# Optimization experiments

Hardware: AMD Instinct MI355X
Metric: run time of the kernel (lower is better)

## Reference

```python
import jax, jax.numpy as jnp
import numpy as np

B, S, V, D, H, DK, DFF, L = 2, 1024, 513, 512, 8, 64, 2048, 6
PAD_IDX = -1.0
EPS_GPE = 0.1

def _sinusoid_table(n_position, d_hid):
    pos = np.arange(n_position)[:, None].astype(np.float64)
    i = np.arange(d_hid)[None, :]
    angle = pos / np.power(10000.0, 2 * (i // 2) / d_hid)
    tab = np.zeros((n_position, d_hid), dtype=np.float32)
    tab[:, 0::2] = np.sin(angle[:, 0::2])
    tab[:, 1::2] = np.cos(angle[:, 1::2])
    return jnp.asarray(tab)

_POS_TABLE = _sinusoid_table(2048, D)

def _ln(x, g, b, eps=1e-6):
    m = x.mean(-1, keepdims=True)
    v = x.var(-1, keepdims=True)
    return (x - m) * jax.lax.rsqrt(v + eps) * g + b

def _mha(x_q, x_kv, wq_, wk_, wv_, wo_, mask, g, b):
    Bq, Sq, _ = x_q.shape
    Skv = x_kv.shape[1]
    q = (x_q @ wq_).reshape(Bq, Sq, H, DK).transpose(0, 2, 1, 3)
    k = (x_kv @ wk_).reshape(Bq, Skv, H, DK).transpose(0, 2, 1, 3)
    v = (x_kv @ wv_).reshape(Bq, Skv, H, DK).transpose(0, 2, 1, 3)
    scores = jnp.einsum('bhqd,bhkd->bhqk', q, k) / np.float32(np.sqrt(DK))
    scores = jnp.where(mask[:, None], scores, jnp.float32(-1e9))
    attn = jax.nn.softmax(scores, axis=-1)
    out = jnp.einsum('bhqk,bhkd->bhqd', attn, v).transpose(0, 2, 1, 3).reshape(Bq, Sq, D)
    return _ln(x_q + out @ wo_, g, b)

def _forward(dec_in, prev_dec_out, trg, adj, graph_length, gr_mask, gr_pos_enc_kernel,
             emb_w1, emb_b1, emb_w2, emb_b2, emb_w3, emb_b3, ln0_g, ln0_b,
             wq, wk, wv, wo, ln1_g, ln1_b,
             cq, ck, cv, co, ln2_g, ln2_b,
             ffn_w1, ffn_b1, ffn_w2, ffn_b2, ln3_g, ln3_b,
             p_w1, p_b1, p_w2, p_b2, p_w3, p_b3):
    # masks (n_ensemble = 1 so dec_in[:, :, 0, :] == dec_in)
    causal = jnp.tril(jnp.ones((S, S), bool))
    slf_mask = jnp.all(dec_in != PAD_IDX, -1)[:, None, :] & causal          # [B,S,S]
    enc_mask = jnp.all(prev_dec_out != PAD_IDX, -1)[:, None, :]             # [B,1,S]
    # word-embedding MLP: 513 -> 513 -> 513 -> 512
    h = jax.nn.relu(dec_in @ emb_w1 + emb_b1)
    h = jax.nn.relu(h @ emb_w2 + emb_b2)
    h = h @ emb_w3 + emb_b3                                                 # [B,S,D]
    # propagation graph positional encoding (k = 0..2, un-normalized branch)
    w = (1.0 - EPS_GPE) ** jnp.arange(gr_pos_enc_kernel.shape[1], dtype=jnp.float32)
    base = _POS_TABLE[:S]                                                   # [S,D]
    emb = jnp.einsum('k,bkst,td->bsd', w, gr_pos_enc_kernel, base) / w.sum()
    h = _ln(h + emb, ln0_g, ln0_b)
    for i in range(L):
        h = _mha(h, h, wq[i], wk[i], wv[i], wo[i], slf_mask, ln1_g[i], ln1_b[i])
        h = _mha(h, prev_dec_out, cq[i], ck[i], cv[i], co[i], enc_mask, ln2_g[i], ln2_b[i])
        f = jax.nn.relu(h @ ffn_w1[i] + ffn_b1[i]) @ ffn_w2[i] + ffn_b2[i]
        h = _ln(h + f, ln3_g[i], ln3_b[i])
    # projection head: 512 -> 513 -> 513 -> 513
    z = jax.nn.relu(h @ p_w1 + p_b1)
    z = jax.nn.relu(z @ p_w2 + p_b2)
    return z @ p_w3 + p_b3                                                  # [B,S,V]

def setup_inputs():
    key = jax.random.key(0)
    ks = jax.random.split(key, 24)
    def xavier(k, shape):
        lim = np.float32(np.sqrt(6.0 / (shape[-2] + shape[-1])))
        return jax.random.uniform(k, shape, jnp.float32, -lim, lim)
    inp = {}
    inp['dec_in'] = jax.random.uniform(ks[0], (B, S, V), jnp.float32)
    inp['prev_dec_out'] = jax.random.normal(ks[1], (B, S, D), jnp.float32)
    inp['trg'] = jnp.zeros((B, S, V), jnp.float32)
    inp['adj'] = jnp.zeros((B, S, S), jnp.float32)
    inp['graph_length'] = jnp.zeros((B, S, 10), jnp.float32)
    inp['gr_mask'] = jnp.zeros((B, 1, S, S), jnp.float32)
    gk = jax.random.uniform(ks[2], (B, 3, S, S), jnp.float32)
    inp['gr_pos_enc_kernel'] = gk / jnp.sum(gk, -1, keepdims=True)  # row-stochastic diffusion kernels
    SZ = max(V, D)  # sz_intermed = 513
    inp['emb_w1'] = xavier(ks[3], (V, SZ)); inp['emb_b1'] = jnp.zeros((SZ,))
    inp['emb_w2'] = xavier(ks[4], (SZ, SZ)); inp['emb_b2'] = jnp.zeros((SZ,))
    inp['emb_w3'] = xavier(ks[5], (SZ, D)); inp['emb_b3'] = jnp.zeros((D,))
    inp['ln0_g'] = jnp.ones((D,)); inp['ln0_b'] = jnp.zeros((D,))
    for name, ki, shp in [('wq', 6, (L, D, D)), ('wk', 7, (L, D, D)), ('wv', 8, (L, D, D)), ('wo', 9, (L, D, D)),
                          ('cq', 10, (L, D, D)), ('ck', 11, (L, D, D)), ('cv', 12, (L, D, D)), ('co', 13, (L, D, D)),
                          ('ffn_w1', 14, (L, D, DFF)), ('ffn_w2', 15, (L, DFF, D))]:
        inp[name] = xavier(ks[ki], shp)
    inp['ffn_b1'] = jnp.zeros((L, DFF)); inp['ffn_b2'] = jnp.zeros((L, D))
    inp['ln1_g'] = jnp.ones((L, D)); inp['ln1_b'] = jnp.zeros((L, D))
    inp['ln2_g'] = jnp.ones((L, D)); inp['ln2_b'] = jnp.zeros((L, D))
    inp['ln3_g'] = jnp.ones((L, D)); inp['ln3_b'] = jnp.zeros((L, D))
    inp['p_w1'] = xavier(ks[16], (D, V)); inp['p_b1'] = jnp.zeros((V,))
    inp['p_w2'] = xavier(ks[17], (V, V)); inp['p_b2'] = jnp.zeros((V,))
    inp['p_w3'] = xavier(ks[18], (V, V)); inp['p_b3'] = jnp.zeros((V,))
    return inp

def reference(dec_in, prev_dec_out, trg, adj, graph_length, gr_mask, gr_pos_enc_kernel,
              emb_w1, emb_b1, emb_w2, emb_b2, emb_w3, emb_b3, ln0_g, ln0_b,
              wq, wk, wv, wo, ln1_g, ln1_b,
              cq, ck, cv, co, ln2_g, ln2_b,
              ffn_w1, ffn_b1, ffn_w2, ffn_b2, ln3_g, ln3_b,
              p_w1, p_b1, p_w2, p_b2, p_w3, p_b3):
    return _forward(dec_in, prev_dec_out, trg, adj, graph_length, gr_mask, gr_pos_enc_kernel,
                    emb_w1, emb_b1, emb_w2, emb_b2, emb_w3, emb_b3, ln0_g, ln0_b,
                    wq, wk, wv, wo, ln1_g, ln1_b,
                    cq, ck, cv, co, ln2_g, ln2_b,
                    ffn_w1, ffn_b1, ffn_w2, ffn_b2, ln3_g, ln3_b,
                    p_w1, p_b1, p_w2, p_b2, p_w3, p_b3)
```

## Files before the change

kernel.cpp:

```cpp
#include <hip/hip_runtime.h>
#include <hip/hip_bf16.h>
#include <stdint.h>

#define BB 2
#define SS 1024
#define VV 513
#define VP 576
#define DD 512
#define HH 8
#define DKK 64
#define DFFN 2048
#define LL 6
#define MM (BB * SS)

typedef __bf16 bf16x8 __attribute__((ext_vector_type(8)));
typedef float f32x4 __attribute__((ext_vector_type(4)));
typedef unsigned short us8 __attribute__((ext_vector_type(8)));
typedef unsigned short us4 __attribute__((ext_vector_type(4)));

static __device__ inline unsigned short f2bf(float f) {
  union { float f; unsigned u; } v; v.f = f;
  unsigned u = v.u;
  unsigned r = (u + 0x7FFFu + ((u >> 16) & 1u)) >> 16;
  return (unsigned short)r;
}

static __device__ inline bf16x8 ldfrag(const unsigned short* p) {
  us8 r = *(const us8*)p;
  return __builtin_bit_cast(bf16x8, r);
}

typedef __attribute__((address_space(3))) void lds_void;
typedef const __attribute__((address_space(1))) void glb_void;
static __device__ inline void gl_lds16(const void* g, void* l) {
  __builtin_amdgcn_global_load_lds((glb_void*)g, (lds_void*)l, 16, 0, 0);
}

static __device__ inline bf16x8 ldfrag_swz(const unsigned short* base, int row, int kloc) {
  const unsigned byte = (unsigned)(row * 128 + kloc * 2) ^ (unsigned)((row & 7) << 4);
  return ldfrag((const unsigned short*)((const char*)base + byte));
}

static __device__ inline int rot3(int x) { return (x == 2) ? 0 : x + 1; }

struct GemmP {
  const unsigned short* A;
  const unsigned short* B0; const unsigned short* B1; const unsigned short* B2;
  const float* bias;
  float* C;
  unsigned short* D0; unsigned short* D1; unsigned short* D2;
  int Kp, Np, ldc, Nreal, relu;
};

template<int NB, int NT, int TRV, int KS>
__global__ __launch_bounds__(256)
void gemm_tpl(GemmP p)
{
  constexpr int FN = NT / 32;
  __shared__ unsigned short Al[3][64 * 64];
  __shared__ unsigned short Bl[3][NT * 64];
  const int tid = threadIdx.x;
  const int l = tid & 63, w = tid >> 6;
  const int wm = w >> 1, wn = w & 1;
  const int lr = l & 15, lg = l >> 4;

  const int nbn = p.Np / NT;
  int sel = 0, bx = blockIdx.x;
  if (NB > 1) { sel = bx / nbn; bx -= sel * nbn; }
  const unsigned short* Bmat = p.B0;
  if (NB > 1 && sel == 1) Bmat = p.B1;
  if (NB > 2 && sel == 2) Bmat = p.B2;
  const int m0 = blockIdx.y << 6, n0 = bx * NT;
  const int kz = (KS > 1) ? blockIdx.z : 0;

  f32x4 acc[2][FN];
  const f32x4 zf = {0.f, 0.f, 0.f, 0.f};
#pragma unroll
  for (int i = 0; i < 2; ++i)
#pragma unroll
    for (int j = 0; j < FN; ++j) acc[i][j] = zf;

  const size_t Kp = (size_t)p.Kp;
  const unsigned short* Abase = p.A + (size_t)m0 * Kp;
  const unsigned short* Bbase = Bmat + (size_t)n0 * Kp;
  const int nt = (p.Kp >> 6) / KS;
  const int kb0 = kz * nt;

  auto stage = [&](int buf, int kt) {
    const int k0 = (kb0 + kt) << 6;
#pragma unroll
    for (int j = 0; j < 2; ++j) {
      const int ti = j * 256 + tid;
      const int row = ti >> 3;
      const int ch = (ti & 7) ^ (row & 7);
      gl_lds16(Abase + (size_t)row * Kp + k0 + ch * 8, &Al[buf][ti * 8]);
    }
#pragma unroll
    for (int j = 0; j < FN; ++j) {
      const int ti = j * 256 + tid;
      const int row = ti >> 3;
      const int ch = (ti & 7) ^ (row & 7);
      gl_lds16(Bbase + (size_t)row * Kp + k0 + ch * 8, &Bl[buf][ti * 8]);
    }
  };

  stage(0, 0);
  if (nt > 1) stage(1, 1);
  int cb = 0, sb = 2;

  for (int kt = 0; kt < nt; ++kt) {
    if (kt + 1 < nt) {
      if constexpr (FN == 2) asm volatile("s_waitcnt vmcnt(4)" ::: "memory");
      else                   asm volatile("s_waitcnt vmcnt(6)" ::: "memory");
    } else {
      asm volatile("s_waitcnt vmcnt(0)" ::: "memory");
    }
    __builtin_amdgcn_s_barrier();
    if (kt + 2 < nt) { stage(sb, kt + 2); sb = rot3(sb); }
#pragma unroll
    for (int ks = 0; ks < 2; ++ks) {
      bf16x8 af[2], bfv[FN];
#pragma unroll
      for (int mf = 0; mf < 2; ++mf)
        af[mf] = ldfrag_swz(Al[cb], wm * 32 + mf * 16 + lr, ks * 32 + lg * 8);
#pragma unroll
      for (int nf = 0; nf < FN; ++nf)
        bfv[nf] = ldfrag_swz(Bl[cb], wn * (NT / 2) + nf * 16 + lr, ks * 32 + lg * 8);
#pragma unroll
      for (int mf = 0; mf < 2; ++mf)
#pragma unroll
        for (int nf = 0; nf < FN; ++nf)
          acc[mf][nf] = __builtin_amdgcn_mfma_f32_16x16x32_bf16(af[mf], bfv[nf], acc[mf][nf], 0, 0, 0);
    }
    cb = rot3(cb);
  }

  unsigned short* Dsel = p.D0;
  if (NB > 1 && sel == 1) Dsel = p.D1;
  if (NB > 2 && sel == 2) Dsel = p.D2;

  if (TRV && sel == 2) {
#pragma unroll
    for (int mf = 0; mf < 2; ++mf) {
      const int growb = m0 + wm * 32 + mf * 16 + (lg << 2);
      const int b = growb >> 10, s = growb & 1023;
#pragma unroll
      for (int nf = 0; nf < FN; ++nf) {
        const int gcol = n0 + wn * (NT / 2) + nf * 16 + lr;
        const int h = gcol >> 6, d = gcol & 63;
        us4 t;
#pragma unroll
        for (int r = 0; r < 4; ++r) t[r] = f2bf(acc[mf][nf][r]);
        *(us4*)(Dsel + (((size_t)(b * HH) + h) * DKK + d) * SS + s) = t;
      }
    }
    return;
  }

  float* Cz = p.C ? (p.C + (size_t)kz * MM * p.ldc) : nullptr;
#pragma unroll
  for (int mf = 0; mf < 2; ++mf) {
#pragma unroll
    for (int r = 0; r < 4; ++r) {
      const int grow = m0 + wm * 32 + mf * 16 + (lg << 2) + r;
#pragma unroll
      for (int nf = 0; nf < FN; ++nf) {
        const int gcol = n0 + wn * (NT / 2) + nf * 16 + lr;
        float v = acc[mf][nf][r];
        if (p.bias && kz == 0 && gcol < p.Nreal) v += p.bias[gcol];
        if (p.relu) v = fmaxf(v, 0.f);
        if (Dsel) Dsel[(size_t)grow * p.Np + gcol] = f2bf(v);
        if (Cz && gcol < p.Nreal) Cz[(size_t)grow * p.ldc + gcol] = v;
      }
    }
  }
}

struct GemmBat {
  const unsigned short* A;
  const unsigned short* B[12];
  unsigned short* D[12];
  int Kp, Np;
};

__global__ __launch_bounds__(256)
void gemm_bat(GemmBat p)
{
  __shared__ unsigned short Al[3][64 * 64];
  __shared__ unsigned short Bl[3][64 * 64];
  const int tid = threadIdx.x;
  const int l = tid & 63, w = tid >> 6;
  const int wm = w >> 1, wn = w & 1;
  const int lr = l & 15, lg = l >> 4;

  const int nbn = p.Np >> 6;
  const int sel = blockIdx.x / nbn;
  const int bx = blockIdx.x - sel * nbn;
  const unsigned short* Bmat = p.B[sel];
  unsigned short* Dmat = p.D[sel];
  const int m0 = blockIdx.y << 6, n0 = bx << 6;

  f32x4 acc[2][2];
  const f32x4 zf = {0.f, 0.f, 0.f, 0.f};
#pragma unroll
  for (int i = 0; i < 2; ++i)
#pragma unroll
    for (int j = 0; j < 2; ++j) acc[i][j] = zf;

  const size_t Kp = (size_t)p.Kp;
  const unsigned short* Abase = p.A + (size_t)m0 * Kp;
  const unsigned short* Bbase = Bmat + (size_t)n0 * Kp;

  auto stage = [&](int buf, int kt) {
    const int k0 = kt << 6;
#pragma unroll
    for (int j = 0; j < 2; ++j) {
      const int ti = j * 256 + tid;
      const int row = ti >> 3;
      const int ch = (ti & 7) ^ (row & 7);
      gl_lds16(Abase + (size_t)row * Kp + k0 + ch * 8, &Al[buf][ti * 8]);
    }
#pragma unroll
    for (int j = 0; j < 2; ++j) {
      const int ti = j * 256 + tid;
      const int row = ti >> 3;
      const int ch = (ti & 7) ^ (row & 7);
      gl_lds16(Bbase + (size_t)row * Kp + k0 + ch * 8, &Bl[buf][ti * 8]);
    }
  };

  const int nt = p.Kp >> 6;
  stage(0, 0);
  if (nt > 1) stage(1, 1);
  int cb = 0, sb = 2;

  for (int kt = 0; kt < nt; ++kt) {
    if (kt + 1 < nt) asm volatile("s_waitcnt vmcnt(4)" ::: "memory");
    else             asm volatile("s_waitcnt vmcnt(0)" ::: "memory");
    __builtin_amdgcn_s_barrier();
    if (kt + 2 < nt) { stage(sb, kt + 2); sb = rot3(sb); }
#pragma unroll
    for (int ks = 0; ks < 2; ++ks) {
      bf16x8 af[2], bfv[2];
#pragma unroll
      for (int mf = 0; mf < 2; ++mf)
        af[mf] = ldfrag_swz(Al[cb], wm * 32 + mf * 16 + lr, ks * 32 + lg * 8);
#pragma unroll
      for (int nf = 0; nf < 2; ++nf)
        bfv[nf] = ldfrag_swz(Bl[cb], wn * 32 + nf * 16 + lr, ks * 32 + lg * 8);
#pragma unroll
      for (int mf = 0; mf < 2; ++mf)
#pragma unroll
        for (int nf = 0; nf < 2; ++nf)
          acc[mf][nf] = __builtin_amdgcn_mfma_f32_16x16x32_bf16(af[mf], bfv[nf], acc[mf][nf], 0, 0, 0);
    }
    cb = rot3(cb);
  }

  if (sel & 1) {
#pragma unroll
    for (int mf = 0; mf < 2; ++mf) {
      const int growb = m0 + wm * 32 + mf * 16 + (lg << 2);
      const int b = growb >> 10, s = growb & 1023;
#pragma unroll
      for (int nf = 0; nf < 2; ++nf) {
        const int gcol = n0 + wn * 32 + nf * 16 + lr;
        const int h = gcol >> 6, d = gcol & 63;
        us4 t;
#pragma unroll
        for (int r = 0; r < 4; ++r) t[r] = f2bf(acc[mf][nf][r]);
        *(us4*)(Dmat + (((size_t)(b * HH) + h) * DKK + d) * SS + s) = t;
      }
    }
    return;
  }

#pragma unroll
  for (int mf = 0; mf < 2; ++mf) {
#pragma unroll
    for (int r = 0; r < 4; ++r) {
      const int grow = m0 + wm * 32 + mf * 16 + (lg << 2) + r;
#pragma unroll
      for (int nf = 0; nf < 2; ++nf) {
        const int gcol = n0 + wn * 32 + nf * 16 + lr;
        Dmat[(size_t)grow * p.Np + gcol] = f2bf(acc[mf][nf][r]);
      }
    }
  }
}

__global__ __launch_bounds__(128)
void attn_kernel(const unsigned short* __restrict__ Qb,
                 const unsigned short* __restrict__ Kb,
                 const unsigned short* __restrict__ VbT,
                 unsigned short* __restrict__ Ob,
                 const float* __restrict__ maskadd)
{
  __shared__ unsigned short Kl[2][2][64 * 64];
  __shared__ unsigned short Vl[2][2][64 * 64];
  __shared__ char PC[9216];
  unsigned short* Pl = (unsigned short*)PC;
  float (*comb)[66] = (float(*)[66])PC;

  const int tid = threadIdx.x;
  const int l = tid & 63, w = tid >> 6;
  const int qt = blockIdx.x, h = blockIdx.y, b = blockIdx.z;
  const int lr = l & 15, lg = l >> 4;

  bf16x8 qf[2][2];
#pragma unroll
  for (int mf = 0; mf < 2; ++mf) {
    const unsigned short* qrow = Qb + ((size_t)(b * SS) + qt * 32 + mf * 16 + lr) * DD + h * DKK;
    qf[mf][0] = ldfrag(qrow + (lg << 3));
    qf[mf][1] = ldfrag(qrow + 32 + (lg << 3));
  }

  const unsigned short* Kbase = Kb + (size_t)(b * SS) * DD + h * DKK;
  const unsigned short* Vbase = VbT + ((size_t)(b * HH) + h) * DKK * SS;

  auto stage = [&](int buf, int kt) {
#pragma unroll
    for (int j = 0; j < 8; ++j) {
      const int ti = j * 64 + l;
      const int row = ti >> 3;
      const int ch = (ti & 7) ^ (row & 7);
      gl_lds16(Kbase + (size_t)(kt * 64 + row) * DD + ch * 8, &Kl[w][buf][ti * 8]);
    }
#pragma unroll
    for (int j = 0; j < 8; ++j) {
      const int ti = j * 64 + l;
      const int row = ti >> 3;
      const int ch = (ti & 7) ^ (row & 7);
      gl_lds16(Vbase + (size_t)row * SS + kt * 64 + ch * 8, &Vl[w][buf][ti * 8]);
    }
  };

  f32x4 accO[2][4];
  const f32x4 zf = {0.f, 0.f, 0.f, 0.f};
#pragma unroll
  for (int mf = 0; mf < 2; ++mf)
#pragma unroll
    for (int nf = 0; nf < 4; ++nf) accO[mf][nf] = zf;
  float mold[2][4], lsum[2][4];
#pragma unroll
  for (int mf = 0; mf < 2; ++mf)
#pragma unroll
    for (int r = 0; r < 4; ++r) { mold[mf][r] = -1e30f; lsum[mf][r] = 0.f; }

  const int ktmax = (qt >> 1) + 1;
  const int myn = (ktmax - w + 1) >> 1;

  if (myn > 0) stage(0, w);
  int buf = 0;

  for (int i = 0; i < myn; ++i) {
    const int kt = w + 2 * i;
    if (i + 1 < myn) {
      stage(buf ^ 1, kt + 2);
      asm volatile("s_waitcnt vmcnt(16)" ::: "memory");
    } else {
      asm volatile("s_waitcnt vmcnt(0)" ::: "memory");
    }
    const unsigned short* KB = &Kl[w][buf][0];
    const unsigned short* VB = &Vl[w][buf][0];
    float sc[2][4][4];
    __builtin_amdgcn_s_setprio(1);
#pragma unroll
    for (int nf = 0; nf < 4; ++nf) {
      bf16x8 k0 = ldfrag_swz(KB, nf * 16 + lr, lg * 8);
      bf16x8 k1 = ldfrag_swz(KB, nf * 16 + lr, 32 + lg * 8);
// ... 309 lines not shown
        accO[mf][nf] = __builtin_amdgcn_mfma_f32_16x16x32_bf16(pa[mf][1], v1, accO[mf][nf], 0, 0, 0);
      }
    }
    __builtin_amdgcn_s_setprio(0);
    buf ^= 1;
  }

  __syncthreads();
  if (w == 1) {
#pragma unroll
    for (int mf = 0; mf < 2; ++mf)
#pragma unroll
      for (int r = 0; r < 4; ++r) {
        const int qrow = mf * 16 + (lg << 2) + r;
#pragma unroll
        for (int nf = 0; nf < 4; ++nf)
          comb[qrow][nf * 16 + lr] = accO[mf][nf][r];
        if (lr == 0) { comb[qrow][64] = mold[mf][r]; comb[qrow][65] = lsum[mf][r]; }
      }
  }
  __syncthreads();
  if (w == 0) {
#pragma unroll
    for (int mf = 0; mf < 2; ++mf)
#pragma unroll
      for (int r = 0; r < 4; ++r) {
        const int qrow = mf * 16 + (lg << 2) + r;
        const float m1 = comb[qrow][64], l1 = comb[qrow][65];
        const float m0v = mold[mf][r], l0 = lsum[mf][r];
        const float ms = fmaxf(m0v, m1);
        const float f0 = __expf(m0v - ms), f1 = __expf(m1 - ms);
        const float inv = 1.f / (l0 * f0 + l1 * f1);
        const size_t orow = ((size_t)(b * SS) + qt * 32 + mf * 16 + (lg << 2) + r) * DD + h * DKK;
#pragma unroll
        for (int nf = 0; nf < 4; ++nf)
          Ob[orow + nf * 16 + lr] =
              f2bf((accO[mf][nf][r] * f0 + comb[qrow][nf * 16 + lr] * f1) * inv);
      }
  }
}

template<int P>
__global__ __launch_bounds__(256)
void addln_kernel(const float* __restrict__ a, const float* __restrict__ c,
                  const float* __restrict__ g, const float* __restrict__ bb,
                  float* __restrict__ hf, unsigned short* __restrict__ hb)
{
  const int row = blockIdx.x * 4 + (threadIdx.x >> 6);
  const int l = threadIdx.x & 63;
  const float* ar = a + (size_t)row * DD + l * 8;
  f32x4 x0 = *(const f32x4*)ar;
  f32x4 x1 = *(const f32x4*)(ar + 4);
#pragma unroll
  for (int pp = 0; pp < P; ++pp) {
    const float* cr = c + (size_t)pp * MM * DD + (size_t)row * DD + l * 8;
    x0 += *(const f32x4*)cr;
    x1 += *(const f32x4*)(cr + 4);
  }
  float sum = x0[0] + x0[1] + x0[2] + x0[3] + x1[0] + x1[1] + x1[2] + x1[3];
#pragma unroll
  for (int off = 1; off < 64; off <<= 1) sum += __shfl_xor(sum, off, 64);
  const float mean = sum * (1.f / 512.f);
  float vs = 0.f;
#pragma unroll
  for (int j = 0; j < 4; ++j) { float d0 = x0[j] - mean; float d1 = x1[j] - mean; vs += d0 * d0 + d1 * d1; }
#pragma unroll
  for (int off = 1; off < 64; off <<= 1) vs += __shfl_xor(vs, off, 64);
  const float rs = rsqrtf(vs * (1.f / 512.f) + 1e-6f);
  const f32x4 g0 = *(const f32x4*)(g + l * 8), g1 = *(const f32x4*)(g + l * 8 + 4);
  const f32x4 b0 = *(const f32x4*)(bb + l * 8), b1 = *(const f32x4*)(bb + l * 8 + 4);
  f32x4 o0, o1;
  us8 ob;
#pragma unroll
  for (int j = 0; j < 4; ++j) {
    o0[j] = (x0[j] - mean) * rs * g0[j] + b0[j];
    o1[j] = (x1[j] - mean) * rs * g1[j] + b1[j];
    ob[j] = f2bf(o0[j]); ob[j + 4] = f2bf(o1[j]);
  }
  float* of = hf + (size_t)row * DD + l * 8;
  *(f32x4*)of = o0; *(f32x4*)(of + 4) = o1;
  *(us8*)(hb + (size_t)row * DD + l * 8) = ob;
}

__global__ __launch_bounds__(256)
void prep_all(const float* __restrict__ dec_in, const float* __restrict__ prev,
              unsigned short* __restrict__ decb, unsigned short* __restrict__ prevb,
              float* __restrict__ kvs, float* __restrict__ kve,
              unsigned short* __restrict__ tabT,
              const float* __restrict__ gk, unsigned short* __restrict__ Mb)
{
  const int blk = blockIdx.x, tid = threadIdx.x;
  if (blk < 1024) {
    const int isdec = blk < 512;
    const int row = (isdec ? blk : blk - 512) * 4 + (tid >> 6);
    const int l = tid & 63;
    const int NC = isdec ? VV : DD, NP = isdec ? VP : DD;
    const float* xr = (isdec ? dec_in : prev) + (size_t)row * NC;
    unsigned short* ob = (isdec ? decb : prevb) + (size_t)row * NP;
    int ok = 1;
    for (int j = l; j < NP; j += 64) {
      if (j < NC) {
        const float v = xr[j];
        ok &= (v != -1.0f) ? 1 : 0;
        ob[j] = f2bf(v);
      } else ob[j] = 0;
    }
    ok = __all(ok) ? 1 : 0;
    if (l == 0) (isdec ? kvs : kve)[row] = ok ? 0.f : -1e9f;
  } else if (blk < 3072) {
    const int i = (blk - 1024) * 256 + tid;
    const int d = i >> 10, s = i & 1023;
    const float ex = (float)(2 * (d >> 1)) * (1.0f / (float)DD);
    const float ang = (float)s * exp2f(ex * -13.287712379549449f);
    tabT[i] = f2bf((d & 1) ? cosf(ang) : sinf(ang));
  } else {
    const int i = (blk - 3072) * 256 + tid;
    const int b = i / (SS * SS);
    const int rem = i - b * (SS * SS);
    const float* p = gk + (size_t)b * 3 * SS * SS + rem;
    Mb[i] = f2bf((p[0] + 0.9f * p[SS * SS] + 0.81f * p[2 * SS * SS]) * (1.0f / 2.71f));
  }
}

struct WJobs {
  const float* W[8]; unsigned short* WT[8];
  int K[8], N[8], Kp[8], Np[8], nbx[8], nby[8];
  int off[9];
};
__global__ __launch_bounds__(256)
void wconv_all(WJobs p)
{
  __shared__ float t[64][65];
  const int bid = blockIdx.x;
  int j = 0;
#pragma unroll
  for (int i = 0; i < 8; ++i) if (bid >= p.off[i + 1]) j = i + 1;
  const int local = bid - p.off[j];
  const int per = p.nbx[j] * p.nby[j];
  const int z = local / per;
  const int rem = local - z * per;
  const int by = rem / p.nbx[j];
  const int bx = rem - by * p.nbx[j];
  const int K = p.K[j], N = p.N[j], Kp = p.Kp[j], Np = p.Np[j];
  const float* Wl = p.W[j] + (size_t)z * K * N;
  unsigned short* WTl = p.WT[j] + (size_t)z * Np * Kp;
  const int n0 = bx << 6, k0 = by << 6;
  const int cx = threadIdx.x & 63, ry = threadIdx.x >> 6;
#pragma unroll
  for (int i = 0; i < 16; ++i) {
    const int kk = k0 + ry + i * 4, nn = n0 + cx;
    t[ry + i * 4][cx] = (kk < K && nn < N) ? Wl[(size_t)kk * N + nn] : 0.f;
  }
  __syncthreads();
#pragma unroll
  for (int i = 0; i < 16; ++i) {
    const int nn = n0 + ry + i * 4, kk = k0 + cx;
    if (nn < Np && kk < Kp) WTl[(size_t)nn * Kp + kk] = f2bf(t[cx][ry + i * 4]);
  }
}

struct WconvB { const float* W[8]; unsigned short* WT[8]; };
__global__ __launch_bounds__(256)
void wconv8_kernel(WconvB p)
{
  __shared__ float t[64][65];
  const int z = blockIdx.z;
  const int wi = z / LL, li = z - wi * LL;
  const float* Wl = p.W[wi] + (size_t)li * DD * DD;
  unsigned short* WTl = p.WT[wi] + (size_t)li * DD * DD;
  const int n0 = blockIdx.x << 6, k0 = blockIdx.y << 6;
  const int cx = threadIdx.x & 63, ry = threadIdx.x >> 6;
#pragma unroll
  for (int i = 0; i < 16; ++i)
    t[ry + i * 4][cx] = Wl[(size_t)(k0 + ry + i * 4) * DD + n0 + cx];
  __syncthreads();
#pragma unroll
  for (int i = 0; i < 16; ++i)
    WTl[(size_t)(n0 + ry + i * 4) * DD + k0 + cx] = f2bf(t[cx][ry + i * 4]);
}

static inline void g1(hipStream_t s, const unsigned short* A, const unsigned short* B,
                      const float* bias, float* C, unsigned short* D,
                      int Kp, int Np, int ldc, int Nreal, int relu)
{
  GemmP p{};
  p.A = A; p.B0 = B; p.bias = bias; p.C = C; p.D0 = D;
  p.Kp = Kp; p.Np = Np; p.ldc = ldc; p.Nreal = Nreal; p.relu = relu;
  gemm_tpl<1, 64, 0, 1><<<dim3(Np >> 6, MM >> 6), 256, 0, s>>>(p);
}

static inline void g1w(hipStream_t s, const unsigned short* A, const unsigned short* B,
                       const float* bias, unsigned short* D, int Kp, int Np, int relu)
{
  GemmP p{};
  p.A = A; p.B0 = B; p.bias = bias; p.D0 = D;
  p.Kp = Kp; p.Np = Np; p.ldc = Np; p.Nreal = Np; p.relu = relu;
  gemm_tpl<1, 128, 0, 1><<<dim3(Np >> 7, MM >> 6), 256, 0, s>>>(p);
}

template<int KS>
static inline void g1k(hipStream_t s, const unsigned short* A, const unsigned short* B,
                       const float* bias, float* C, int Kp)
{
  GemmP p{};
  p.A = A; p.B0 = B; p.bias = bias; p.C = C;
  p.Kp = Kp; p.Np = DD; p.ldc = DD; p.Nreal = DD; p.relu = 0;
  gemm_tpl<1, 64, 0, KS><<<dim3(DD >> 6, MM >> 6, KS), 256, 0, s>>>(p);
}

static inline void g3t(hipStream_t s, const unsigned short* A, const unsigned short* B0,
                       const unsigned short* B1, const unsigned short* B2,
                       unsigned short* D0, unsigned short* D1, unsigned short* D2T)
{
  GemmP p{};
  p.A = A; p.B0 = B0; p.B1 = B1; p.B2 = B2; p.D0 = D0; p.D1 = D1; p.D2 = D2T;
  p.Kp = DD; p.Np = DD; p.ldc = DD; p.Nreal = DD; p.relu = 0;
  gemm_tpl<3, 64, 1, 1><<<dim3(3 * (DD >> 6), MM >> 6), 256, 0, s>>>(p);
}

extern "C" void kernel_launch(void* const* d_in, const int* in_sizes, int n_in,
                              void* d_out, int out_size, void* d_ws, size_t ws_size,
                              hipStream_t stream)
{
  (void)in_sizes; (void)n_in; (void)out_size; (void)ws_size;
  const float* dec_in = (const float*)d_in[0];
  const float* prev   = (const float*)d_in[1];
  const float* gk     = (const float*)d_in[6];
  const float* emb_w1 = (const float*)d_in[7];
  const float* emb_b1 = (const float*)d_in[8];
  const float* emb_w2 = (const float*)d_in[9];
  const float* emb_b2 = (const float*)d_in[10];
  const float* emb_w3 = (const float*)d_in[11];
  const float* emb_b3 = (const float*)d_in[12];
  const float* ln0_g  = (const float*)d_in[13];
  const float* ln0_b  = (const float*)d_in[14];
  const float* wq     = (const float*)d_in[15];
  const float* wk     = (const float*)d_in[16];
  const float* wv     = (const float*)d_in[17];
  const float* wo     = (const float*)d_in[18];
  const float* cq     = (const float*)d_in[19];
  const float* ck     = (const float*)d_in[20];
  const float* cv     = (const float*)d_in[21];
  const float* co     = (const float*)d_in[22];
  const float* ffn_w1 = (const float*)d_in[23];
  const float* ffn_w2 = (const float*)d_in[24];
  const float* ffn_b1 = (const float*)d_in[25];
  const float* ffn_b2 = (const float*)d_in[26];
  const float* ln1_g  = (const float*)d_in[27];
  const float* ln1_b  = (const float*)d_in[28];
  const float* ln2_g  = (const float*)d_in[29];
  const float* ln2_b  = (const float*)d_in[30];
  const float* ln3_g  = (const float*)d_in[31];
  const float* ln3_b  = (const float*)d_in[32];
  const float* p_w1   = (const float*)d_in[33];
  const float* p_b1   = (const float*)d_in[34];
  const float* p_w2   = (const float*)d_in[35];
  const float* p_b2   = (const float*)d_in[36];
  const float* p_w3   = (const float*)d_in[37];
  const float* p_b3   = (const float*)d_in[38];

  char* wsp = (char*)d_ws;
  auto carve = [&](size_t bytes) { char* r = wsp; wsp += (bytes + 255) & ~(size_t)255; return r; };

  unsigned short* decb  = (unsigned short*)carve((size_t)MM * VP * 2);
  unsigned short* prevb = (unsigned short*)carve((size_t)MM * DD * 2);
  float*          hf    = (float*)carve((size_t)MM * DD * 4);
  unsigned short* hb    = (unsigned short*)carve((size_t)MM * DD * 2);
  float*          xf1   = (float*)carve((size_t)MM * DD * 4);
  unsigned short* tb1   = (unsigned short*)carve((size_t)MM * DFFN * 2);
  unsigned short* Mbb   = tb1;
  float*          xf2   = (float*)((char*)tb1 + (size_t)MM * SS * 2);
  unsigned short* tb2a  = (unsigned short*)carve((size_t)MM * VP * 2);
  unsigned short* tb2b  = (unsigned short*)carve((size_t)MM * VP * 2);
  unsigned short* qb    = (unsigned short*)carve((size_t)MM * DD * 2);
  unsigned short* kb    = (unsigned short*)carve((size_t)MM * DD * 2);
  unsigned short* vbT   = (unsigned short*)carve((size_t)MM * DD * 2);
  float* kvs = (float*)carve((size_t)MM * 4);
  float* kve = (float*)carve((size_t)MM * 4);
  unsigned short* postabt = (unsigned short*)carve((size_t)DD * SS * 2);
  unsigned short* ew1t  = (unsigned short*)carve((size_t)VP * VP * 2);
  unsigned short* ew2t  = (unsigned short*)carve((size_t)VP * VP * 2);
  unsigned short* ew3t  = (unsigned short*)carve((size_t)DD * VP * 2);
  unsigned short* wqt   = (unsigned short*)carve((size_t)LL * DD * DD * 2);
  unsigned short* wkt   = (unsigned short*)carve((size_t)LL * DD * DD * 2);
  unsigned short* wvt   = (unsigned short*)carve((size_t)LL * DD * DD * 2);
  unsigned short* wot   = (unsigned short*)carve((size_t)LL * DD * DD * 2);
  unsigned short* cqt   = (unsigned short*)carve((size_t)LL * DD * DD * 2);
  unsigned short* ckt   = (unsigned short*)carve((size_t)LL * DD * DD * 2);
  unsigned short* cvt   = (unsigned short*)carve((size_t)LL * DD * DD * 2);
  unsigned short* cot   = (unsigned short*)carve((size_t)LL * DD * DD * 2);
  unsigned short* f1t   = (unsigned short*)carve((size_t)LL * DFFN * DD * 2);
  unsigned short* f2t   = (unsigned short*)carve((size_t)LL * DD * DFFN * 2);
  unsigned short* p1t   = (unsigned short*)carve((size_t)VP * DD * 2);
  unsigned short* p2t   = (unsigned short*)carve((size_t)VP * VP * 2);
  unsigned short* p3t   = (unsigned short*)carve((size_t)VP * VP * 2);
  unsigned short* ckall = (unsigned short*)carve((size_t)LL * MM * DD * 2);
  unsigned short* cvbT  = (unsigned short*)carve((size_t)LL * MM * DD * 2);
  float*          xk4   = (float*)carve((size_t)4 * MM * DD * 4);

  const dim3 agrid(SS / 32, HH, BB);

  prep_all<<<11264, 256, 0, stream>>>(dec_in, prev, decb, prevb, kvs, kve, postabt, gk, Mbb);

  {
    WconvB wb{};
    wb.W[0] = wq; wb.W[1] = wk; wb.W[2] = wv; wb.W[3] = wo;
    wb.W[4] = cq; wb.W[5] = ck; wb.W[6] = cv; wb.W[7] = co;
    wb.WT[0] = wqt; wb.WT[1] = wkt; wb.WT[2] = wvt; wb.WT[3] = wot;
    wb.WT[4] = cqt; wb.WT[5] = ckt; wb.WT[6] = cvt; wb.WT[7] = cot;
    wconv8_kernel<<<dim3(8, 8, 8 * LL), 256, 0, stream>>>(wb);
  }
  {
    WJobs wj{};
    const float* Ws[8]   = {emb_w1, emb_w2, emb_w3, ffn_w1, ffn_w2, p_w1, p_w2, p_w3};
    unsigned short* Ds[8] = {ew1t, ew2t, ew3t, f1t, f2t, p1t, p2t, p3t};
    const int Ks[8]  = {VV, VV, VV, DD, DFFN, DD, VV, VV};
    const int Ns[8]  = {VV, VV, DD, DFFN, DD, VV, VV, VV};
    const int Kps[8] = {VP, VP, VP, DD, DFFN, DD, VP, VP};
    const int Nps[8] = {VP, VP, DD, DFFN, DD, VP, VP, VP};
    const int nls[8] = {1, 1, 1, LL, LL, 1, 1, 1};
    int off = 0;
    for (int j = 0; j < 8; ++j) {
      wj.W[j] = Ws[j]; wj.WT[j] = Ds[j];
      wj.K[j] = Ks[j]; wj.N[j] = Ns[j]; wj.Kp[j] = Kps[j]; wj.Np[j] = Nps[j];
      wj.nbx[j] = (Nps[j] + 63) / 64; wj.nby[j] = (Kps[j] + 63) / 64;
      wj.off[j] = off;
      off += wj.nbx[j] * wj.nby[j] * nls[j];
    }
    wj.off[8] = off;
    wconv_all<<<off, 256, 0, stream>>>(wj);
  }

  {
    GemmBat p{};
    p.A = prevb; p.Kp = DD; p.Np = DD;
    for (int i = 0; i < LL; ++i) {
      p.B[2 * i]     = ckt + (size_t)i * DD * DD;
      p.B[2 * i + 1] = cvt + (size_t)i * DD * DD;
      p.D[2 * i]     = ckall + (size_t)i * MM * DD;
      p.D[2 * i + 1] = cvbT + (size_t)i * MM * DD;
    }
    gemm_bat<<<dim3(12 * (DD >> 6), MM >> 6), 256, 0, stream>>>(p);
  }

  g1(stream, decb, ew1t, emb_b1, nullptr, tb2a, VP, VP, VP, VV, 1);
  g1(stream, tb2a, ew2t, emb_b2, nullptr, tb2b, VP, VP, VP, VV, 1);
  g1(stream, tb2b, ew3t, emb_b3, xf1, nullptr, VP, DD, DD, DD, 0);
  g1(stream, Mbb, postabt, nullptr, xf2, nullptr, SS, DD, DD, DD, 0);
  addln_kernel<1><<<MM / 4, 256, 0, stream>>>(xf1, xf2, ln0_g, ln0_b, hf, hb);

  for (int i = 0; i < LL; ++i) {
    const size_t od = (size_t)i * DD * DD;
    g3t(stream, hb, wqt + od, wkt + od, wvt + od, qb, kb, vbT);
    attn_kernel<<<agrid, 128, 0, stream>>>(qb, kb, vbT, qb, kvs);
    g1k<2>(stream, qb, wot + od, nullptr, xk4, DD);
    addln_kernel<2><<<MM / 4, 256, 0, stream>>>(hf, xk4, ln1_g + i * DD, ln1_b + i * DD, hf, hb);
    attnx_kernel<<<agrid, 128, 0, stream>>>(hb, cqt + od, ckall + (size_t)i * MM * DD,
                                            cvbT + (size_t)i * MM * DD, qb, kve);
    g1k<2>(stream, qb, cot + od, nullptr, xk4, DD);
    addln_kernel<2><<<MM / 4, 256, 0, stream>>>(hf, xk4, ln2_g + i * DD, ln2_b + i * DD, hf, hb);
    g1w(stream, hb, f1t + (size_t)i * DFFN * DD, ffn_b1 + i * DFFN, tb1, DD, DFFN, 1);
    g1k<4>(stream, tb1, f2t + (size_t)i * DD * DFFN, ffn_b2 + i * DD, xk4, DFFN);
    addln_kernel<4><<<MM / 4, 256, 0, stream>>>(hf, xk4, ln3_g + i * DD, ln3_b + i * DD, hf, hb);
  }

  g1(stream, hb, p1t, p_b1, nullptr, tb2a, DD, VP, VP, VV, 1);
  g1(stream, tb2a, p2t, p_b2, nullptr, tb2b, VP, VP, VP, VV, 1);
  g1(stream, tb2b, p3t, p_b3, (float*)d_out, nullptr, VP, VP, VV, VV, 0);
}
```

Baseline: 994.0 us.

## Merge prologue kernels and batch independent startup GEMMs into one launch

The input prep, positional table, graph-kernel mix and both weight-transpose kernels are combined into a single prologue launch with block-range dispatch. The cross-attention K/V batch GEMM, the first embedding GEMM and the positional-encoding GEMM are also merged into one multi-job GEMM launch, since they are mutually independent. The aim is to cut launch overhead and the idle gaps at each kernel tail. The cost is a larger shared-memory footprint on every prologue block and hard-coded block counts that assume these exact shapes.

```diff
diff --git a/kernel.cpp b/kernel.cpp
--- a/kernel.cpp
+++ b/kernel.cpp
@@ -43,6 +43,61 @@
 
 static __device__ inline int rot3(int x) { return (x == 2) ? 0 : x + 1; }
 
+__device__ __forceinline__ void gemm_core64(
+    unsigned short* Al, unsigned short* Bl,
+    const unsigned short* Abase, const unsigned short* Bbase, int Kp, int nt,
+    f32x4 (&acc)[2][2])
+{
+  const int tid = threadIdx.x;
+  const int l = tid & 63, w = tid >> 6;
+  const int wm = w >> 1, wn = w & 1;
+  const int lr = l & 15, lg = l >> 4;
+
+  auto stage = [&](int buf, int kt) {
+    const int k0 = kt << 6;
+#pragma unroll
+    for (int j = 0; j < 2; ++j) {
+      const int ti = j * 256 + tid;
+      const int row = ti >> 3;
+      const int ch = (ti & 7) ^ (row & 7);
+      gl_lds16(Abase + (size_t)row * Kp + k0 + ch * 8, &Al[buf * 4096 + ti * 8]);
+    }
+#pragma unroll
+    for (int j = 0; j < 2; ++j) {
+      const int ti = j * 256 + tid;
+      const int row = ti >> 3;
+      const int ch = (ti & 7) ^ (row & 7);
+      gl_lds16(Bbase + (size_t)row * Kp + k0 + ch * 8, &Bl[buf * 4096 + ti * 8]);
+    }
+  };
+
+  stage(0, 0);
+  if (nt > 1) stage(1, 1);
+  int cb = 0, sb = 2;
+  for (int kt = 0; kt < nt; ++kt) {
+    if (kt + 1 < nt) asm volatile("s_waitcnt vmcnt(4)" ::: "memory");
+    else             asm volatile("s_waitcnt vmcnt(0)" ::: "memory");
+    __builtin_amdgcn_s_barrier();
+    if (kt + 2 < nt) { stage(sb, kt + 2); sb = rot3(sb); }
+#pragma unroll
+    for (int ks = 0; ks < 2; ++ks) {
+      bf16x8 af[2], bfv[2];
+#pragma unroll
+      for (int mf = 0; mf < 2; ++mf)
+        af[mf] = ldfrag_swz(Al + cb * 4096, wm * 32 + mf * 16 + lr, ks * 32 + lg * 8);
+#pragma unroll
+      for (int nf = 0; nf < 2; ++nf)
+        bfv[nf] = ldfrag_swz(Bl + cb * 4096, wn * 32 + nf * 16 + lr, ks * 32 + lg * 8);
+#pragma unroll
+      for (int mf = 0; mf < 2; ++mf)
+#pragma unroll
+        for (int nf = 0; nf < 2; ++nf)
+          acc[mf][nf] = __builtin_amdgcn_mfma_f32_16x16x32_bf16(af[mf], bfv[nf], acc[mf][nf], 0, 0, 0);
+    }
+    cb = rot3(cb);
+  }
+}
+
 struct GemmP {
   const unsigned short* A;
   const unsigned short* B0; const unsigned short* B1; const unsigned short* B2;
@@ -176,116 +231,102 @@
   }
 }
 
-struct GemmBat {
+struct GemmMultiP {
   const unsigned short* A;
   const unsigned short* B[12];
   unsigned short* D[12];
-  int Kp, Np;
+  const unsigned short* eA; const unsigned short* eB; const float* ebias;
+  unsigned short* eD;
+  const unsigned short* gA; const unsigned short* gB; float* gC;
 };
 
 __global__ __launch_bounds__(256)
-void gemm_bat(GemmBat p)
-{
-  __shared__ unsigned short Al[3][64 * 64];
-  __shared__ unsigned short Bl[3][64 * 64];
+void gemm_multi(GemmMultiP p)
+{
+  __shared__ unsigned short Al[3 * 4096];
+  __shared__ unsigned short Bl[3 * 4096];
+  const int bid = blockIdx.x;
   const int tid = threadIdx.x;
   const int l = tid & 63, w = tid >> 6;
   const int wm = w >> 1, wn = w & 1;
   const int lr = l & 15, lg = l >> 4;
-
-  const int nbn = p.Np >> 6;
-  const int sel = blockIdx.x / nbn;
-  const int bx = blockIdx.x - sel * nbn;
-  const unsigned short* Bmat = p.B[sel];
-  unsigned short* Dmat = p.D[sel];
-  const int m0 = blockIdx.y << 6, n0 = bx << 6;
-
+  const f32x4 zf = {0.f, 0.f, 0.f, 0.f};
   f32x4 acc[2][2];
-  const f32x4 zf = {0.f, 0.f, 0.f, 0.f};
 #pragma unroll
   for (int i = 0; i < 2; ++i)
 #pragma unroll
     for (int j = 0; j < 2; ++j) acc[i][j] = zf;
 
-  const size_t Kp = (size_t)p.Kp;
-  const unsigned short* Abase = p.A + (size_t)m0 * Kp;
-  const unsigned short* Bbase = Bmat + (size_t)n0 * Kp;
-
-  auto stage = [&](int buf, int kt) {
-    const int k0 = kt << 6;
-#pragma unroll
-    for (int j = 0; j < 2; ++j) {
-      const int ti = j * 256 + tid;
-      const int row = ti >> 3;
-      const int ch = (ti & 7) ^ (row & 7);
-      gl_lds16(Abase + (size_t)row * Kp + k0 + ch * 8, &Al[buf][ti * 8]);
-    }
-#pragma unroll
-    for (int j = 0; j < 2; ++j) {
-      const int ti = j * 256 + tid;
-      const int row = ti >> 3;
-      const int ch = (ti & 7) ^ (row & 7);
-      gl_lds16(Bbase + (size_t)row * Kp + k0 + ch * 8, &Bl[buf][ti * 8]);
-    }
-  };
-
-  const int nt = p.Kp >> 6;
-  stage(0, 0);
-  if (nt > 1) stage(1, 1);
-  int cb = 0, sb = 2;
-
-  for (int kt = 0; kt < nt; ++kt) {
-    if (kt + 1 < nt) asm volatile("s_waitcnt vmcnt(4)" ::: "memory");
-    else             asm volatile("s_waitcnt vmcnt(0)" ::: "memory");
-    __builtin_amdgcn_s_barrier();
-    if (kt + 2 < nt) { stage(sb, kt + 2); sb = rot3(sb); }
-#pragma unroll
-    for (int ks = 0; ks < 2; ++ks) {
-      bf16x8 af[2], bfv[2];
+  if (bid < 3072) {
+    const int sel = bid >> 8;
+    const int rem = bid & 255;
+    const int by = rem >> 3, bx = rem & 7;
+    const int m0 = by << 6, n0 = bx << 6;
+    gemm_core64(Al, Bl, p.A + (size_t)m0 * DD, p.B[sel] + (size_t)n0 * DD, DD, 8, acc);
+    unsigned short* Dmat = p.D[sel];
+    if (sel & 1) {
+#pragma unroll
+      for (int mf = 0; mf < 2; ++mf) {
+        const int growb = m0 + wm * 32 + mf * 16 + (lg << 2);
+        const int b = growb >> 10, s = growb & 1023;
+#pragma unroll
+        for (int nf = 0; nf < 2; ++nf) {
+          const int gcol = n0 + wn * 32 + nf * 16 + lr;
+          const int h = gcol >> 6, d = gcol & 63;
+          us4 t;
+#pragma unroll
+          for (int r = 0; r < 4; ++r) t[r] = f2bf(acc[mf][nf][r]);
+          *(us4*)(Dmat + (((size_t)(b * HH) + h) * DKK + d) * SS + s) = t;
+        }
+      }
+    } else {
 #pragma unroll
       for (int mf = 0; mf < 2; ++mf)
-        af[mf] = ldfrag_swz(Al[cb], wm * 32 + mf * 16 + lr, ks * 32 + lg * 8);
-#pragma unroll
-      for (int nf = 0; nf < 2; ++nf)
-        bfv[nf] = ldfrag_swz(Bl[cb], wn * 32 + nf * 16 + lr, ks * 32 + lg * 8);
-#pragma unroll
-      for (int mf = 0; mf < 2; ++mf)
-#pragma unroll
-        for (int nf = 0; nf < 2; ++nf)
-          acc[mf][nf] = __builtin_amdgcn_mfma_f32_16x16x32_bf16(af[mf], bfv[nf], acc[mf][nf], 0, 0, 0);
-    }
-    cb = rot3(cb);
-  }
-
-  if (sel & 1) {
-#pragma unroll
-    for (int mf = 0; mf < 2; ++mf) {
-      const int growb = m0 + wm * 32 + mf * 16 + (lg << 2);
-      const int b = growb >> 10, s = growb & 1023;
-#pragma unroll
-      for (int nf = 0; nf < 2; ++nf) {
-        const int gcol = n0 + wn * 32 + nf * 16 + lr;
-        const int h = gcol >> 6, d = gcol & 63;
-        us4 t;
-#pragma unroll
-        for (int r = 0; r < 4; ++r) t[r] = f2bf(acc[mf][nf][r]);
-        *(us4*)(Dmat + (((size_t)(b * HH) + h) * DKK + d) * SS + s) = t;
-      }
-    }
-    return;
-  }
-
-#pragma unroll
-  for (int mf = 0; mf < 2; ++mf) {
-#pragma unroll
-    for (int r = 0; r < 4; ++r) {
-      const int grow = m0 + wm * 32 + mf * 16 + (lg << 2) + r;
-#pragma unroll
-      for (int nf = 0; nf < 2; ++nf) {
-        const int gcol = n0 + wn * 32 + nf * 16 + lr;
-        Dmat[(size_t)grow * p.Np + gcol] = f2bf(acc[mf][nf][r]);
-      }
-    }
+#pragma unroll
+        for (int r = 0; r < 4; ++r) {
+          const int grow = m0 + wm * 32 + mf * 16 + (lg << 2) + r;
+#pragma unroll
+          for (int nf = 0; nf < 2; ++nf) {
+            const int gcol = n0 + wn * 32 + nf * 16 + lr;
+            Dmat[(size_t)grow * DD + gcol] = f2bf(acc[mf][nf][r]);
+          }
+        }
+    }
+  } else if (bid < 3360) {
+    const int local = bid - 3072;
+    const int by = local / 9, bx = local - by * 9;
+    const int m0 = by << 6, n0 = bx << 6;
+    gemm_core64(Al, Bl, p.eA + (size_t)m0 * VP, p.eB + (size_t)n0 * VP, VP, 9, acc);
+#pragma unroll
+    for (int mf = 0; mf < 2; ++mf)
+#pragma unroll
+      for (int r = 0; r < 4; ++r) {
+        const int grow = m0 + wm * 32 + mf * 16 + (lg << 2) + r;
+#pragma unroll
+        for (int nf = 0; nf < 2; ++nf) {
+          const int gcol = n0 + wn * 32 + nf * 16 + lr;
+          float v = acc[mf][nf][r];
+          if (gcol < VV) v += p.ebias[gcol];
+          v = fmaxf(v, 0.f);
+          p.eD[(size_t)grow * VP + gcol] = f2bf(v);
+        }
+      }
+  } else {
+    const int local = bid - 3360;
+    const int by = local >> 3, bx = local & 7;
+    const int m0 = by << 6, n0 = bx << 6;
+    gemm_core64(Al, Bl, p.gA + (size_t)m0 * SS, p.gB + (size_t)n0 * SS, SS, 16, acc);
+#pragma unroll
+    for (int mf = 0; mf < 2; ++mf)
+#pragma unroll
+      for (int r = 0; r < 4; ++r) {
+        const int grow = m0 + wm * 32 + mf * 16 + (lg << 2) + r;
+#pragma unroll
+        for (int nf = 0; nf < 2; ++nf) {
+          const int gcol = n0 + wn * 32 + nf * 16 + lr;
+          p.gC[(size_t)grow * DD + gcol] = acc[mf][nf][r];
+        }
+      }
   }
 }
 
@@ -761,21 +802,28 @@
   *(us8*)(hb + (size_t)row * DD + l * 8) = ob;
 }
 
+struct ProP {
+  const float *dec_in, *prev, *gk;
+  unsigned short *decb, *prevb, *tabT, *Mb;
+  float *kvs, *kve;
+  const float* W8[8]; unsigned short* WT8[8];
+  const float* W[8]; unsigned short* WT[8];
+  int K[8], N[8], Kp[8], Np[8], nbx[8], nby[8];
+  int off[9];
+};
+
 __global__ __launch_bounds__(256)
-void prep_all(const float* __restrict__ dec_in, const float* __restrict__ prev,
-              unsigned short* __restrict__ decb, unsigned short* __restrict__ prevb,
-              float* __restrict__ kvs, float* __restrict__ kve,
-              unsigned short* __restrict__ tabT,
-              const float* __restrict__ gk, unsigned short* __restrict__ Mb)
-{
-  const int blk = blockIdx.x, tid = threadIdx.x;
-  if (blk < 1024) {
-    const int isdec = blk < 512;
-    const int row = (isdec ? blk : blk - 512) * 4 + (tid >> 6);
+void prologue_all(ProP p)
+{
+  __shared__ float t[64][65];
+  const int bid = blockIdx.x, tid = threadIdx.x;
+  if (bid < 1024) {
+    const int isdec = bid < 512;
+    const int row = (isdec ? bid : bid - 512) * 4 + (tid >> 6);
     const int l = tid & 63;
     const int NC = isdec ? VV : DD, NP = isdec ? VP : DD;
-    const float* xr = (isdec ? dec_in : prev) + (size_t)row * NC;
-    unsigned short* ob = (isdec ? decb : prevb) + (size_t)row * NP;
+    const float* xr = (isdec ? p.dec_in : p.prev) + (size_t)row * NC;
+    unsigned short* ob = (isdec ? p.decb : p.prevb) + (size_t)row * NP;
     int ok = 1;
     for (int j = l; j < NP; j += 64) {
       if (j < NC) {
@@ -785,77 +833,64 @@
       } else ob[j] = 0;
     }
     ok = __all(ok) ? 1 : 0;
-    if (l == 0) (isdec ? kvs : kve)[row] = ok ? 0.f : -1e9f;
-  } else if (blk < 3072) {
-    const int i = (blk - 1024) * 256 + tid;
+    if (l == 0) (isdec ? p.kvs : p.kve)[row] = ok ? 0.f : -1e9f;
+  } else if (bid < 3072) {
+    const int i = (bid - 1024) * 256 + tid;
     const int d = i >> 10, s = i & 1023;
     const float ex = (float)(2 * (d >> 1)) * (1.0f / (float)DD);
     const float ang = (float)s * exp2f(ex * -13.287712379549449f);
-    tabT[i] = f2bf((d & 1) ? cosf(ang) : sinf(ang));
-  } else {
-    const int i = (blk - 3072) * 256 + tid;
+    p.tabT[i] = f2bf((d & 1) ? cosf(ang) : sinf(ang));
+  } else if (bid < 11264) {
+    const int i = (bid - 3072) * 256 + tid;
     const int b = i / (SS * SS);
     const int rem = i - b * (SS * SS);
-    const float* p = gk + (size_t)b * 3 * SS * SS + rem;
-    Mb[i] = f2bf((p[0] + 0.9f * p[SS * SS] + 0.81f * p[2 * SS * SS]) * (1.0f / 2.71f));
-  }
-}
-
-struct WJobs {
-  const float* W[8]; unsigned short* WT[8];
-  int K[8], N[8], Kp[8], Np[8], nbx[8], nby[8];
-  int off[9];
-};
-__global__ __launch_bounds__(256)
-void wconv_all(WJobs p)
-{
-  __shared__ float t[64][65];
-  const int bid = blockIdx.x;
-  int j = 0;
-#pragma unroll
-  for (int i = 0; i < 8; ++i) if (bid >= p.off[i + 1]) j = i + 1;
-  const int local = bid - p.off[j];
-  const int per = p.nbx[j] * p.nby[j];
-  const int z = local / per;
-  const int rem = local - z * per;
-  const int by = rem / p.nbx[j];
-  const int bx = rem - by * p.nbx[j];
-  const int K = p.K[j], N = p.N[j], Kp = p.Kp[j], Np = p.Np[j];
-  const float* Wl = p.W[j] + (size_t)z * K * N;
-  unsigned short* WTl = p.WT[j] + (size_t)z * Np * Kp;
-  const int n0 = bx << 6, k0 = by << 6;
-  const int cx = threadIdx.x & 63, ry = threadIdx.x >> 6;
-#pragma unroll
-  for (int i = 0; i < 16; ++i) {
-    const int kk = k0 + ry + i * 4, nn = n0 + cx;
-    t[ry + i * 4][cx] = (kk < K && nn < N) ? Wl[(size_t)kk * N + nn] : 0.f;
-  }
-  __syncthreads();
-#pragma unroll
-  for (int i = 0; i < 16; ++i) {
-    const int nn = n0 + ry + i * 4, kk = k0 + cx;
-    if (nn < Np && kk < Kp) WTl[(size_t)nn * Kp + kk] = f2bf(t[cx][ry + i * 4]);
-  }
-}
-
-struct WconvB { const float* W[8]; unsigned short* WT[8]; };
-__global__ __launch_bounds__(256)
-void wconv8_kernel(WconvB p)
-{
-  __shared__ float t[64][65];
-  const int z = blockIdx.z;
-  const int wi = z / LL, li = z - wi * LL;
-  const float* Wl = p.W[wi] + (size_t)li * DD * DD;
-  unsigned short* WTl = p.WT[wi] + (size_t)li * DD * DD;
-  const int n0 = blockIdx.x << 6, k0 = blockIdx.y << 6;
-  const int cx = threadIdx.x & 63, ry = threadIdx.x >> 6;
-#pragma unroll
-  for (int i = 0; i < 16; ++i)
-    t[ry + i * 4][cx] = Wl[(size_t)(k0 + ry + i * 4) * DD + n0 + cx];
-  __syncthreads();
-#pragma unroll
-  for (int i = 0; i < 16; ++i)
-    WTl[(size_t)(n0 + ry + i * 4) * DD + k0 + cx] = f2bf(t[cx][ry + i * 4]);
+    const float* q = p.gk + (size_t)b * 3 * SS * SS + rem;
+    p.Mb[i] = f2bf((q[0] + 0.9f * q[SS * SS] + 0.81f * q[2 * SS * SS]) * (1.0f / 2.71f));
+  } else if (bid < 11264 + 3072) {
+    const int idx = bid - 11264;
+    const int z = idx >> 6;
+    const int rem = idx & 63;
+    const int by = rem >> 3, bx = rem & 7;
+    const int wi = z / LL, li = z - wi * LL;
+    const float* Wl = p.W8[wi] + (size_t)li * DD * DD;
+    unsigned short* WTl = p.WT8[wi] + (size_t)li * DD * DD;
+    const int n0 = bx << 6, k0 = by << 6;
+    const int cx = tid & 63, ry = tid >> 6;
+#pragma unroll
+    for (int i = 0; i < 16; ++i)
+      t[ry + i * 4][cx] = Wl[(size_t)(k0 + ry + i * 4) * DD + n0 + cx];
+    __syncthreads();
+#pragma unroll
+    for (int i = 0; i < 16; ++i)
+      WTl[(size_t)(n0 + ry + i * 4) * DD + k0 + cx] = f2bf(t[cx][ry + i * 4]);
+  } else {
+    const int bid2 = bid - 11264 - 3072;
+    int j = 0;
+#pragma unroll
+    for (int i = 0; i < 8; ++i) if (bid2 >= p.off[i + 1]) j = i + 1;
+    const int local = bid2 - p.off[j];
+    const int per = p.nbx[j] * p.nby[j];
+    const int z = local / per;
+    const int rem = local - z * per;
+    const int by = rem / p.nbx[j];
+    const int bx = rem - by * p.nbx[j];
+    const int K = p.K[j], N = p.N[j], Kp = p.Kp[j], Np = p.Np[j];
+    const float* Wl = p.W[j] + (size_t)z * K * N;
+    unsigned short* WTl = p.WT[j] + (size_t)z * Np * Kp;
+    const int n0 = bx << 6, k0 = by << 6;
+    const int cx = tid & 63, ry = tid >> 6;
+#pragma unroll
+    for (int i = 0; i < 16; ++i) {
+      const int kk = k0 + ry + i * 4, nn = n0 + cx;
+      t[ry + i * 4][cx] = (kk < K && nn < N) ? Wl[(size_t)kk * N + nn] : 0.f;
+    }
+    __syncthreads();
+#pragma unroll
+    for (int i = 0; i < 16; ++i) {
+      const int nn = n0 + ry + i * 4, kk = k0 + cx;
+      if (nn < Np && kk < Kp) WTl[(size_t)nn * Kp + kk] = f2bf(t[cx][ry + i * 4]);
+    }
+  }
 }
 
 static inline void g1(hipStream_t s, const unsigned short* A, const unsigned short* B,
@@ -979,19 +1014,15 @@
 
   const dim3 agrid(SS / 32, HH, BB);
 
-  prep_all<<<11264, 256, 0, stream>>>(dec_in, prev, decb, prevb, kvs, kve, postabt, gk, Mbb);
-
   {
-    WconvB wb{};
-    wb.W[0] = wq; wb.W[1] = wk; wb.W[2] = wv; wb.W[3] = wo;
-    wb.W[4] = cq; wb.W[5] = ck; wb.W[6] = cv; wb.W[7] = co;
-    wb.WT[0] = wqt; wb.WT[1] = wkt; wb.WT[2] = wvt; wb.WT[3] = wot;
-    wb.WT[4] = cqt; wb.WT[5] = ckt; wb.WT[6] = cvt; wb.WT[7] = cot;
-    wconv8_kernel<<<dim3(8, 8, 8 * LL), 256, 0, stream>>>(wb);
-  }
-  {
-    WJobs wj{};
-    const float* Ws[8]   = {emb_w1, emb_w2, emb_w3, ffn_w1, ffn_w2, p_w1, p_w2, p_w3};
+    ProP pp{};
+    pp.dec_in = dec_in; pp.prev = prev; pp.gk = gk;
+    pp.decb = decb; pp.prevb = prevb; pp.tabT = postabt; pp.Mb = Mbb;
+    pp.kvs = kvs; pp.kve = kve;
+    const float* W8s[8] = {wq, wk, wv, wo, cq, ck, cv, co};
+    unsigned short* WT8s[8] = {wqt, wkt, wvt, wot, cqt, ckt, cvt, cot};
+    for (int i = 0; i < 8; ++i) { pp.W8[i] = W8s[i]; pp.WT8[i] = WT8s[i]; }
+    const float* Ws[8]    = {emb_w1, emb_w2, emb_w3, ffn_w1, ffn_w2, p_w1, p_w2, p_w3};
     unsigned short* Ds[8] = {ew1t, ew2t, ew3t, f1t, f2t, p1t, p2t, p3t};
     const int Ks[8]  = {VV, VV, VV, DD, DFFN, DD, VV, VV};
     const int Ns[8]  = {VV, VV, DD, DFFN, DD, VV, VV, VV};
@@ -1000,32 +1031,32 @@
     const int nls[8] = {1, 1, 1, LL, LL, 1, 1, 1};
     int off = 0;
     for (int j = 0; j < 8; ++j) {
-      wj.W[j] = Ws[j]; wj.WT[j] = Ds[j];
-      wj.K[j] = Ks[j]; wj.N[j] = Ns[j]; wj.Kp[j] = Kps[j]; wj.Np[j] = Nps[j];
-      wj.nbx[j] = (Nps[j] + 63) / 64; wj.nby[j] = (Kps[j] + 63) / 64;
-      wj.off[j] = off;
-      off += wj.nbx[j] * wj.nby[j] * nls[j];
-    }
-    wj.off[8] = off;
-    wconv_all<<<off, 256, 0, stream>>>(wj);
+      pp.W[j] = Ws[j]; pp.WT[j] = Ds[j];
+      pp.K[j] = Ks[j]; pp.N[j] = Ns[j]; pp.Kp[j] = Kps[j]; pp.Np[j] = Nps[j];
+      pp.nbx[j] = (Nps[j] + 63) / 64; pp.nby[j] = (Kps[j] + 63) / 64;
+      pp.off[j] = off;
+      off += pp.nbx[j] * pp.nby[j] * nls[j];
+    }
+    pp.off[8] = off;
+    prologue_all<<<11264 + 3072 + off, 256, 0, stream>>>(pp);
   }
 
   {
-    GemmBat p{};
-    p.A = prevb; p.Kp = DD; p.Np = DD;
+    GemmMultiP p{};
+    p.A = prevb;
     for (int i = 0; i < LL; ++i) {
       p.B[2 * i]     = ckt + (size_t)i * DD * DD;
       p.B[2 * i + 1] = cvt + (size_t)i * DD * DD;
       p.D[2 * i]     = ckall + (size_t)i * MM * DD;
       p.D[2 * i + 1] = cvbT + (size_t)i * MM * DD;
     }
-    gemm_bat<<<dim3(12 * (DD >> 6), MM >> 6), 256, 0, stream>>>(p);
-  }
-
-  g1(stream, decb, ew1t, emb_b1, nullptr, tb2a, VP, VP, VP, VV, 1);
+    p.eA = decb; p.eB = ew1t; p.ebias = emb_b1; p.eD = tb2a;
+    p.gA = Mbb; p.gB = postabt; p.gC = xf2;
+    gemm_multi<<<3616, 256, 0, stream>>>(p);
+  }
+
   g1(stream, tb2a, ew2t, emb_b2, nullptr, tb2b, VP, VP, VP, VV, 1);
   g1(stream, tb2b, ew3t, emb_b3, xf1, nullptr, VP, DD, DD, DD, 0);
-  g1(stream, Mbb, postabt, nullptr, xf2, nullptr, SS, DD, DD, DD, 0);
   addln_kernel<1><<<MM / 4, 256, 0, stream>>>(xf1, xf2, ln0_g, ln0_b, hf, hb);
 
   for (int i = 0; i < LL; ++i) {
```

Result: faster. 971.5 us (-2.3%).
